# Kernel tuning notes

Measured on AMD Instinct MI355X. Metric: run time of the kernel, lower is better.

The kernel has to match this reference:

```python
import jax, jax.numpy as jnp
import numpy as np

D = 512
H = 8
HD = D // H  # 64
B = 16
N = 64        # seq_len (variable nodes)
S = N + 1     # new_seq (with CLS)
THRESHOLD = 0.5
LN_EPS = 1e-5


def setup_inputs() -> dict:
    key = jax.random.key(0)
    ks = jax.random.split(key, 12)
    s = 0.02
    return {
        "desc_embeddings": jax.random.normal(ks[0], (B, N, D), jnp.float32),
        "name_value_embeddings": jax.random.normal(ks[1], (B, S, D), jnp.float32),
        "w_gt": jax.random.normal(ks[2], (D, D), jnp.float32) * s,
        "b_gt": jnp.zeros((D,), jnp.float32),
        "topology_bias": jnp.zeros((1,), jnp.float32),
        "w_edge1": jax.random.normal(ks[3], (2 * D, D), jnp.float32) * s,
        "b_edge1": jnp.zeros((D,), jnp.float32),
        "ln_gamma": jnp.ones((D,), jnp.float32),
        "ln_beta": jnp.zeros((D,), jnp.float32),
        "w_edge2": jax.random.normal(ks[4], (D, D), jnp.float32) * s,
        "b_edge2": jnp.zeros((D,), jnp.float32),
        "w_q": jax.random.normal(ks[5], (D, D), jnp.float32) * s,
        "b_q": jnp.zeros((D,), jnp.float32),
        "w_k": jax.random.normal(ks[6], (D, D), jnp.float32) * s,
        "b_k": jnp.zeros((D,), jnp.float32),
        "w_v": jax.random.normal(ks[7], (D, D), jnp.float32) * s,
        "b_v": jnp.zeros((D,), jnp.float32),
        "w_attn": jax.random.normal(ks[8], (3 * HD,), jnp.float32) * s,
        "b_attn": jnp.zeros((1,), jnp.float32),
        "w_out": jax.random.normal(ks[9], (D, D), jnp.float32) * s,
        "b_out": jnp.zeros((D,), jnp.float32),
    }


def _layernorm(x, gamma, beta):
    mu = jnp.mean(x, axis=-1, keepdims=True)
    var = jnp.mean(jnp.square(x - mu), axis=-1, keepdims=True)
    return (x - mu) * jax.lax.rsqrt(var + LN_EPS) * gamma + beta


def reference(desc_embeddings, name_value_embeddings, w_gt, b_gt, topology_bias,
              w_edge1, b_edge1, ln_gamma, ln_beta, w_edge2, b_edge2,
              w_q, b_q, w_k, b_k, w_v, b_v, w_attn, b_attn, w_out, b_out):
    b, s, d = name_value_embeddings.shape
    n = s - 1

    # 1. Global topology (projected desc embeddings, cosine sim, sigmoid)
    de = desc_embeddings @ w_gt + b_gt                                   # [B,N,D]
    de_n = de / jnp.linalg.norm(de, axis=-1, keepdims=True)
    global_sim = jnp.einsum('bnd,bmd->bnm', de_n, de_n)
    gt = jax.nn.sigmoid(global_sim + topology_bias)
    # straight-through threshold (frozen=False)
    hard = (gt > THRESHOLD).astype(gt.dtype)
    gA = hard - jax.lax.stop_gradient(gt) + gt

    # 2. Sample-wise similarity over variable tokens
    var = name_value_embeddings[:, 1:, :]
    var_n = var / jnp.linalg.norm(var, axis=-1, keepdims=True)
    sample_sim = jnp.einsum('bnd,bmd->bnm', var_n, var_n)

    # no self-interaction, then graph-conditioned softmax
    gA = gA * (1.0 - jnp.eye(n, dtype=gt.dtype))[None]
    adjacency = jax.nn.softmax(gA * sample_sim, axis=-1)                 # [B,N,N]

    # 4. Edge attributes [B,S,S,2D] and padded adjacency [B,S,S]
    var_edge = jnp.concatenate([
        jnp.broadcast_to(de[:, :, None, :], (b, n, n, d)),
        jnp.broadcast_to(de[:, None, :, :], (b, n, n, d)),
    ], axis=-1)
    cls_edge = jnp.concatenate([de, de], axis=-1)                        # [B,N,2D]
    edge_attr = jnp.zeros((b, s, s, 2 * d), de.dtype)
    edge_attr = edge_attr.at[:, 1:, 1:].set(var_edge)
    edge_attr = edge_attr.at[:, 0, 1:].set(cls_edge)
    edge_attr = edge_attr.at[:, 1:, 0].set(cls_edge)

    new_adj = jnp.zeros((b, s, s), adjacency.dtype)
    new_adj = new_adj.at[:, 1:, 1:].set(adjacency)
    new_adj = new_adj.at[:, 0, 1:].set(1.0)

    # 5. Attention
    q = (name_value_embeddings @ w_q + b_q).reshape(b, s, H, HD).transpose(0, 2, 1, 3)
    k = (name_value_embeddings @ w_k + b_k).reshape(b, s, H, HD).transpose(0, 2, 1, 3)
    v = (name_value_embeddings @ w_v + b_v).reshape(b, s, H, HD).transpose(0, 2, 1, 3)

    # edge MLP: Linear -> LayerNorm -> ReLU -> Linear
    eu = jax.nn.relu(_layernorm(edge_attr @ w_edge1 + b_edge1, ln_gamma, ln_beta)) @ w_edge2 + b_edge2
    eu = eu.reshape(b, s, s, H, HD)                                      # [B,S,S,H,hd]

    # attn_proj(concat([q_i, k_j, e_ij])) decomposed into three dot products
    wq_a, wk_a, we_a = w_attn[:HD], w_attn[HD:2 * HD], w_attn[2 * HD:]
    score_q = jnp.einsum('bhid,d->bhi', q, wq_a)[:, :, :, None]
    score_k = jnp.einsum('bhjd,d->bhj', k, wk_a)[:, :, None, :]
    # edge features are pre-masked by adjacency; linearity lets us mask the score
    score_e = jnp.einsum('bijhd,d->bhij', eu, we_a) * new_adj[:, None]
    attn = score_q + score_k + score_e + b_attn[0]

    attn = attn + jnp.where(new_adj[:, None] == 0, -1e9, 0.0)
    attn = jax.nn.softmax(attn, axis=-1)                                 # [B,H,S,S]
    # dropout p=0 (eval)

    context = jnp.einsum('bhij,bhjd->bhid', attn, v)
    context = context.transpose(0, 2, 1, 3).reshape(b, s, d)
    output = context @ w_out + b_out
    return output, attn
```

## Files before the change

### kernel.cpp

```cpp
#include <hip/hip_runtime.h>
#include <math.h>


constexpr int kD  = 512;
constexpr int kH  = 8;
constexpr int kHD = 64;
constexpr int kB  = 16;
constexpr int kN  = 64;
constexpr int kS  = 65;

typedef short bf16x8 __attribute__((ext_vector_type(8)));
typedef float f32x4  __attribute__((ext_vector_type(4)));

__device__ __forceinline__ float wsum(float x) {
#pragma unroll
  for (int m = 1; m < 64; m <<= 1) x += __shfl_xor(x, m, 64);
  return x;
}
__device__ __forceinline__ float wmax(float x) {
#pragma unroll
  for (int m = 1; m < 64; m <<= 1) x = fmaxf(x, __shfl_xor(x, m, 64));
  return x;
}
__device__ __forceinline__ float osum(float x) {
  x += __shfl_xor(x, 8, 64);
  x += __shfl_xor(x, 16, 64);
  x += __shfl_xor(x, 32, 64);
  return x;
}

__device__ __forceinline__ unsigned short f2bf(float x) {
  unsigned int u = __builtin_bit_cast(unsigned int, x);
  u += 0x7FFFu + ((u >> 16) & 1u);
  return (unsigned short)(u >> 16);
}
__device__ __forceinline__ float bf2f(unsigned short h) {
  return __builtin_bit_cast(float, ((unsigned int)h) << 16);
}
__device__ __forceinline__ unsigned int pk2(unsigned short a, unsigned short b) {
  return (unsigned int)a | ((unsigned int)b << 16);
}

__global__ __launch_bounds__(256) void conv_w(
    const float* __restrict__ w_q, const float* __restrict__ w_k,
    const float* __restrict__ w_v, const float* __restrict__ w_e1,
    const float* __restrict__ w_o, const float* __restrict__ w_gt,
    unsigned short* __restrict__ wt)
{
  __shared__ float T[32][33];
  const int z = blockIdx.z;
  const float* src = (z == 0) ? w_q : (z == 1) ? w_k : (z == 2) ? w_v
                   : (z == 3) ? w_e1 : (z == 4) ? (w_e1 + 262144)
                   : (z == 5) ? w_o : w_gt;
  unsigned short* hi = wt + (size_t)z * 524288;
  unsigned short* lo = hi + 262144;
  const int n0 = blockIdx.x * 32, k0 = blockIdx.y * 32;
  const int tx = threadIdx.x & 31, ty0 = threadIdx.x >> 5;
#pragma unroll
  for (int it = 0; it < 4; ++it) {
    const int ky = ty0 + it * 8;
    T[ky][tx] = src[(size_t)(k0 + ky) * kD + n0 + tx];
  }
  __syncthreads();
#pragma unroll
  for (int it = 0; it < 4; ++it) {
    const int ny = ty0 + it * 8;
    const float x = T[tx][ny];
    const unsigned short h = f2bf(x);
    hi[(size_t)(n0 + ny) * kD + k0 + tx] = h;
    lo[(size_t)(n0 + ny) * kD + k0 + tx] = f2bf(x - bf2f(h));
  }
}

struct MJob { const float* A; const unsigned short* Wh; const unsigned short* Wl;
              const float* bias; float* C; int M; };
struct MJobs { MJob j[4]; };

__global__ __launch_bounds__(256) void gemm_mfma(
    MJobs jobs, int zNorms,
    const float* __restrict__ deN, const float* __restrict__ nvN,
    float* __restrict__ invde, float* __restrict__ invvar)
{
  if ((int)blockIdx.z == zNorms) {
    const int flat = blockIdx.x + gridDim.x * blockIdx.y;
    const int lane = threadIdx.x & 63;
    const int w = threadIdx.x >> 6;
#pragma unroll
    for (int r = 0; r < 4; ++r) {
      const int wid = flat * 16 + w * 4 + r;
      if (wid >= 2 * kB * kN) break;
      const float* row;
      if (wid < kB * kN) {
        row = deN + (size_t)wid * kD;
      } else {
        const int t = wid - kB * kN;
        row = nvN + ((size_t)(t / kN) * kS + 1 + (t % kN)) * kD;
      }
      const float4* r4 = reinterpret_cast<const float4*>(row) + lane * 2;
      const float4 x0 = r4[0], x1 = r4[1];
      float ss = x0.x * x0.x + x0.y * x0.y + x0.z * x0.z + x0.w * x0.w
               + x1.x * x1.x + x1.y * x1.y + x1.z * x1.z + x1.w * x1.w;
      ss = wsum(ss);
      if (lane == 0) {
        const float inv = 1.f / sqrtf(ss);
        if (wid < kB * kN) invde[wid] = inv; else invvar[wid - kB * kN] = inv;
      }
    }
    return;
  }

  const MJob jb = jobs.j[blockIdx.z];
  __shared__ unsigned short Ah[64][40], Al[64][40], Wh[64][40], Wl[64][40];
  const int tid = threadIdx.x;
  const int lane = tid & 63, wv = tid >> 6;
  const int wr = wv >> 1, wc = wv & 1;
  const int bm = blockIdx.x * 64, bn = blockIdx.y * 64;
  const int sr = tid >> 2, sk = (tid & 3) * 8;
  const bool aok = (bm + sr) < jb.M;
  const float* Ap = jb.A + (size_t)(bm + sr) * kD + sk;
  const unsigned short* Whp = jb.Wh + (size_t)(bn + sr) * kD + sk;
  const unsigned short* Wlp = jb.Wl + (size_t)(bn + sr) * kD + sk;

  const f32x4 zero = {0.f, 0.f, 0.f, 0.f};
  f32x4 acc00 = zero, acc01 = zero, acc10 = zero, acc11 = zero;

  for (int k0 = 0; k0 < kD; k0 += 32) {
    float4 a0 = {0.f, 0.f, 0.f, 0.f}, a1 = {0.f, 0.f, 0.f, 0.f};
    if (aok) {
      a0 = *reinterpret_cast<const float4*>(Ap + k0);
      a1 = *reinterpret_cast<const float4*>(Ap + k0 + 4);
    }
    const uint4 wh4 = *reinterpret_cast<const uint4*>(Whp + k0);
    const uint4 wl4 = *reinterpret_cast<const uint4*>(Wlp + k0);
    const float av[8] = {a0.x, a0.y, a0.z, a0.w, a1.x, a1.y, a1.z, a1.w};
    unsigned short h[8], l[8];
#pragma unroll
    for (int e = 0; e < 8; ++e) {
      h[e] = f2bf(av[e]);
      l[e] = f2bf(av[e] - bf2f(h[e]));
    }
    const uint4 hp = { pk2(h[0], h[1]), pk2(h[2], h[3]), pk2(h[4], h[5]), pk2(h[6], h[7]) };
    const uint4 lp = { pk2(l[0], l[1]), pk2(l[2], l[3]), pk2(l[4], l[5]), pk2(l[6], l[7]) };
    *reinterpret_cast<uint4*>(&Ah[sr][sk]) = hp;
    *reinterpret_cast<uint4*>(&Al[sr][sk]) = lp;
    *reinterpret_cast<uint4*>(&Wh[sr][sk]) = wh4;
    *reinterpret_cast<uint4*>(&Wl[sr][sk]) = wl4;
    __syncthreads();

    const int fr = lane & 15, kg = lane >> 4;
#pragma unroll
    for (int fm = 0; fm < 2; ++fm) {
      const int arow = wr * 32 + fm * 16 + fr;
      const bf16x8 amh = *reinterpret_cast<const bf16x8*>(&Ah[arow][kg * 8]);
      const bf16x8 aml = *reinterpret_cast<const bf16x8*>(&Al[arow][kg * 8]);
#pragma unroll
      for (int fn = 0; fn < 2; ++fn) {
        const int wrow = wc * 32 + fn * 16 + fr;
        const bf16x8 bh = *reinterpret_cast<const bf16x8*>(&Wh[wrow][kg * 8]);
        const bf16x8 bl = *reinterpret_cast<const bf16x8*>(&Wl[wrow][kg * 8]);
        f32x4 acc = (fm == 0) ? (fn == 0 ? acc00 : acc01) : (fn == 0 ? acc10 : acc11);
        acc = __builtin_amdgcn_mfma_f32_16x16x32_bf16(amh, bh, acc, 0, 0, 0);
        acc = __builtin_amdgcn_mfma_f32_16x16x32_bf16(amh, bl, acc, 0, 0, 0);
        acc = __builtin_amdgcn_mfma_f32_16x16x32_bf16(aml, bh, acc, 0, 0, 0);
        if (fm == 0) { if (fn == 0) acc00 = acc; else acc01 = acc; }
        else         { if (fn == 0) acc10 = acc; else acc11 = acc; }
      }
    }
    __syncthreads();
  }

  const int rg = lane >> 4, cc = lane & 15;
#pragma unroll
  for (int fm = 0; fm < 2; ++fm) {
#pragma unroll
    for (int fn = 0; fn < 2; ++fn) {
      const f32x4 acc = (fm == 0) ? (fn == 0 ? acc00 : acc01) : (fn == 0 ? acc10 : acc11);
      const int row0 = bm + wr * 32 + fm * 16 + rg * 4;
      const int col  = bn + wc * 32 + fn * 16 + cc;
      const float bb = jb.bias ? jb.bias[col] : 0.f;
#pragma unroll
      for (int e = 0; e < 4; ++e) {
        const int row = row0 + e;
        if (row < jb.M) jb.C[(size_t)row * kD + col] = acc[e] + bb;
      }
    }
  }
}

__global__ __launch_bounds__(512) void graph_prep(
    const float* __restrict__ de, const float* __restrict__ nv,
    const float* __restrict__ invde, const float* __restrict__ invvar,
    const float* __restrict__ topo_p, float* __restrict__ adj,
    const float* __restrict__ q, const float* __restrict__ k,
    const float* __restrict__ w_attn,
    float* __restrict__ sq, float* __restrict__ sk,
    const float* __restrict__ w_edge2, const float* __restrict__ b_edge2,
    unsigned short* __restrict__ w2ph, unsigned short* __restrict__ w2pl,
    float* __restrict__ b2eff)
{
  const int blk = blockIdx.x;
  if (blk < kB * kN) {
    __shared__ float lg[kN];
    const int b = blk >> 6, i = blk & 63;
    const int w = threadIdx.x >> 6, lane = threadIdx.x & 63;
    const int p = lane & 7, oct = lane >> 3;
    const int j = w * 8 + p;
    const float topo = topo_p[0];
    const float4* di = reinterpret_cast<const float4*>(de + ((size_t)b * kN + i) * kD + oct * 64);
    const float4* dj = reinterpret_cast<const float4*>(de + ((size_t)b * kN + j) * kD + oct * 64);
    const float4* vi = reinterpret_cast<const float4*>(nv + ((size_t)b * kS + 1 + i) * kD + oct * 64);
    const float4* vj = reinterpret_cast<const float4*>(nv + ((size_t)b * kS + 1 + j) * kD + oct * 64);
    float g = 0.f, sv = 0.f;
#pragma unroll
    for (int t = 0; t < 16; ++t) {
      const float4 a = di[t], c = dj[t];
      g += a.x * c.x + a.y * c.y + a.z * c.z + a.w * c.w;
      const float4 x = vi[t], y = vj[t];
      sv += x.x * y.x + x.y * y.y + x.z * y.z + x.w * y.w;
    }
    g = osum(g);
    sv = osum(sv);
    if (oct == 0) {
      const float gs = g * invde[b * kN + i] * invde[b * kN + j] + topo;
      const bool hard = (gs > 0.f) && (j != i);
      lg[j] = hard ? sv * invvar[b * kN + i] * invvar[b * kN + j] : 0.f;
    }
    __syncthreads();
    if (threadIdx.x < 64) {
      const float x = lg[lane];
      const float m = wmax(x);
      const float e = expf(x - m);
      const float s = wsum(e);
      adj[((size_t)b * kN + i) * kN + lane] = e / s;
    }
    return;
  }
  if (blk < kB * kN + 33) {
    const int t = (blk - kB * kN) * 512 + threadIdx.x;
    const int total = kB * kS * kH;
    if (t >= 2 * total) return;
    const int which = (t >= total) ? 1 : 0;
    const int r = which ? t - total : t;
    const int h = r % kH, bs = r / kH;
    const float* src = which ? k : q;
    const float* wa = w_attn + which * kHD;
    const float4* row = reinterpret_cast<const float4*>(src + (size_t)bs * kD + h * kHD);
    const float4* w4 = reinterpret_cast<const float4*>(wa);
    float acc = 0.f;
#pragma unroll
    for (int c = 0; c < kHD / 4; ++c) {
      const float4 a = row[c], w = w4[c];
      acc += a.x * w.x + a.y * w.y + a.z * w.z + a.w * w.w;
    }
    (which ? sk : sq)[r] = acc;
    return;
  }
  {
    const int rel = blk - (kB * kN + 33);
    const float4* wa4 = reinterpret_cast<const float4*>(w_attn + 2 * kHD);
    if (rel < 8) {
      const int t = rel * 512 + threadIdx.x;
      const int c = t >> 3, h = t & 7;
      const float4* s4 = reinterpret_cast<const float4*>(w_edge2 + (size_t)c * kD + h * kHD);
      float acc = 0.f;
#pragma unroll
      for (int u = 0; u < kHD / 4; ++u) {
        const float4 a = s4[u], w = wa4[u];
        acc += a.x * w.x + a.y * w.y + a.z * w.z + a.w * w.w;
      }
      const unsigned short hi = f2bf(acc);
      w2ph[h * kD + c] = hi;
      w2pl[h * kD + c] = f2bf(acc - bf2f(hi));
    } else {
      if (threadIdx.x < kH) {
        const int h = threadIdx.x;
        float acc = 0.f;
        for (int d = 0; d < kHD; ++d)
          acc += b_edge2[h * kHD + d] * w_attn[2 * kHD + d];
        b2eff[h] = acc;
      }
      for (int u = threadIdx.x; u < 8 * kD; u += 512) {
        w2ph[8 * kD + u] = 0;
        w2pl[8 * kD + u] = 0;
      }
    }
  }
}

__global__ __launch_bounds__(256) void edge_scores(
    const float* __restrict__ Pp, const float* __restrict__ Qq,
    const float* __restrict__ gamma, const float* __restrict__ beta,
    const unsigned short* __restrict__ w2ph, const unsigned short* __restrict__ w2pl,
    const float* __restrict__ b2eff, float* __restrict__ es)
{
  const int g = blockIdx.x * 4 + (threadIdx.x >> 6);
  const int lane = threadIdx.x & 63;
  const int m = lane & 15, kg = lane >> 4;
  const int base = g * 16;
  const int b = base / (kS * kN);
  const int r0 = base % (kS * kN);
  const int i = r0 / kN, j0 = r0 % kN;
  const int jj = j0 + m;
  const int qrow = b * kN + jj;
  const int prow = (i == 0) ? qrow : (b * kN + i - 1);
  const float* Pr = Pp + (size_t)prow * kD;
  const float* Qr = Qq + (size_t)qrow * kD;

  float s1 = 0.f, s2 = 0.f;
#pragma unroll 4
  for (int s = 0; s < 16; ++s) {
    const int c = s * 32 + kg * 8;
    const float4 pa = *reinterpret_cast<const float4*>(Pr + c);
    const float4 pb = *reinterpret_cast<const float4*>(Pr + c + 4);
    const float4 qa = *reinterpret_cast<const float4*>(Qr + c);
    const float4 qb = *reinterpret_cast<const float4*>(Qr + c + 4);
    const float z0 = pa.x + qa.x, z1 = pa.y + qa.y, z2 = pa.z + qa.z, z3 = pa.w + qa.w;
    const float z4 = pb.x + qb.x, z5 = pb.y + qb.y, z6 = pb.z + qb.z, z7 = pb.w + qb.w;
    s1 += ((z0 + z1) + (z2 + z3)) + ((z4 + z5) + (z6 + z7));
    s2 += ((z0 * z0 + z1 * z1) + (z2 * z2 + z3 * z3))
        + ((z4 * z4 + z5 * z5) + (z6 * z6 + z7 * z7));
  }
  s1 += __shfl_xor(s1, 16, 64); s1 += __shfl_xor(s1, 32, 64);
  s2 += __shfl_xor(s2, 16, 64); s2 += __shfl_xor(s2, 32, 64);
  const float mu = s1 * (1.f / kD);
  const float var = s2 * (1.f / kD) - mu * mu;
  const float rstd = rsqrtf(var + 1e-5f);
  const float nb = -mu * rstd;

  const f32x4 zero = {0.f, 0.f, 0.f, 0.f};
  f32x4 accA = zero, accB = zero, accC = zero;
#pragma unroll 4
  for (int s = 0; s < 16; ++s) {
    const int c = s * 32 + kg * 8;
    const float4 pa = *reinterpret_cast<const float4*>(Pr + c);
    const float4 pb = *reinterpret_cast<const float4*>(Pr + c + 4);
    const float4 qa = *reinterpret_cast<const float4*>(Qr + c);
    const float4 qb = *reinterpret_cast<const float4*>(Qr + c + 4);
    const float4 ga = *reinterpret_cast<const float4*>(gamma + c);
    const float4 gb = *reinterpret_cast<const float4*>(gamma + c + 4);
    const float4 ba = *reinterpret_cast<const float4*>(beta + c);
    const float4 bb = *reinterpret_cast<const float4*>(beta + c + 4);
    const float zv[8] = { pa.x + qa.x, pa.y + qa.y, pa.z + qa.z, pa.w + qa.w,
                          pb.x + qb.x, pb.y + qb.y, pb.z + qb.z, pb.w + qb.w };
    const float gv[8] = { ga.x, ga.y, ga.z, ga.w, gb.x, gb.y, gb.z, gb.w };
    const float bv[8] = { ba.x, ba.y, ba.z, ba.w, bb.x, bb.y, bb.z, bb.w };
    unsigned short h8[8], l8[8];
#pragma unroll
    for (int e = 0; e < 8; ++e) {
      const float zn = fmaf(zv[e], rstd, nb);
      const float eu = fmaxf(fmaf(zn, gv[e], bv[e]), 0.f);
      h8[e] = f2bf(eu);
      l8[e] = f2bf(eu - bf2f(h8[e]));
    }
    const uint4 hp = { pk2(h8[0], h8[1]), pk2(h8[2], h8[3]), pk2(h8[4], h8[5]), pk2(h8[6], h8[7]) };
    const uint4 lp = { pk2(l8[0], l8[1]), pk2(l8[2], l8[3]), pk2(l8[4], l8[5]), pk2(l8[6], l8[7]) };
    const bf16x8 Af_h = __builtin_bit_cast(bf16x8, hp);
    const bf16x8 Af_l = __builtin_bit_cast(bf16x8, lp);
    const bf16x8 Bh = *reinterpret_cast<const bf16x8*>(w2ph + (size_t)m * kD + c);
    const bf16x8 Bl = *reinterpret_cast<const bf16x8*>(w2pl + (size_t)m * kD + c);
    accA = __builtin_amdgcn_mfma_f32_16x16x32_bf16(Af_h, Bh, accA, 0, 0, 0);
    accB = __builtin_amdgcn_mfma_f32_16x16x32_bf16(Af_h, Bl, accB, 0, 0, 0);
    accC = __builtin_amdgcn_mfma_f32_16x16x32_bf16(Af_l, Bh, accC, 0, 0, 0);
  }

  const int n = lane & 15;
  if (n < kH) {
    const float be = b2eff[n];
#pragma unroll
    for (int e = 0; e < 4; ++e) {
      const int mp = kg * 4 + e;
      es[(((size_t)b * kS + i) * kS + (j0 + mp + 1)) * kH + n]
          = (accA[e] + accB[e]) + accC[e] + be;
    }
  }
}

__global__ __launch_bounds__(576) void attn_ctx(
    const float* __restrict__ sq, const float* __restrict__ sk,
    const float* __restrict__ es, const float* __restrict__ adj,
    const float* __restrict__ v, const float* __restrict__ b_attn,
    float* __restrict__ attn_out, float* __restrict__ ctx)
{
  __shared__ float prob[kH][kS];
  const int bi = blockIdx.x;
  const int b = bi / kS, i = bi % kS;
  const int tid = threadIdx.x;
  const float ba = b_attn[0];
  if (tid < kH * kS) {
    const int h = tid / kS, j = tid % kS;
    float lgv;
    if (j == 0) {
      lgv = -1e30f;
    } else {
      const float a = (i == 0) ? 1.f : adj[((size_t)b * kN + (i - 1)) * kN + (j - 1)];
      lgv = sq[(b * kS + i) * kH + h] + sk[(b * kS + j) * kH + h]
          + es[(((size_t)b * kS + i) * kS + j) * kH + h] * a + ba;
    }
    prob[h][j] = lgv;
  }
  __syncthreads();
  const int w = tid >> 6, lane = tid & 63;
  if (w < kH) {
    const float x = prob[w][lane];
    const float xe = prob[w][64];
    float m = wmax(x);
    m = fmaxf(m, xe);
    const float e = expf(x - m);
    const float ee = expf(xe - m);
    const float s = wsum(e) + ee;
    const float inv = 1.f / s;
    prob[w][lane] = e * inv;
    if (lane == 0) prob[w][64] = ee * inv;
  }
  __syncthreads();
  if (tid < kH * kS) {
    const int h = tid / kS, j = tid % kS;
    attn_out[(((size_t)b * kH + h) * kS + i) * kS + j] = prob[h][j];
  }
  if (tid < kD) {
    const int h = tid >> 6, d = tid & 63;
    const float* vb = v + (size_t)b * kS * kD + h * kHD + d;
    float a0 = 0.f, a1 = 0.f, a2 = 0.f, a3 = 0.f;
#pragma unroll 4
    for (int j = 1; j < kS; j += 4) {
      a0 = fmaf(prob[h][j + 0], vb[(size_t)(j + 0) * kD], a0);
      a1 = fmaf(prob[h][j + 1], vb[(size_t)(j + 1) * kD], a1);
      a2 = fmaf(prob[h][j + 2], vb[(size_t)(j + 2) * kD], a2);
      a3 = fmaf(prob[h][j + 3], vb[(size_t)(j + 3) * kD], a3);
    }
    ctx[((size_t)b * kS + i) * kD + tid] = (a0 + a1) + (a2 + a3);
  }
}

extern "C" void kernel_launch(void* const* d_in, const int* in_sizes, int n_in,
                              void* d_out, int out_size, void* d_ws, size_t ws_size,
                              hipStream_t stream)
{
  const float* desc = (const float*)d_in[0];
  const float* nv   = (const float*)d_in[1];
  const float* w_gt = (const float*)d_in[2];
  const float* b_gt = (const float*)d_in[3];
  const float* topo = (const float*)d_in[4];
  const float* w_e1 = (const float*)d_in[5];
  const float* b_e1 = (const float*)d_in[6];
  const float* ln_g = (const float*)d_in[7];
  const float* ln_b = (const float*)d_in[8];
  const float* w_e2 = (const float*)d_in[9];
  const float* b_e2 = (const float*)d_in[10];
  const float* w_q  = (const float*)d_in[11];
  const float* b_q  = (const float*)d_in[12];
  const float* w_k  = (const float*)d_in[13];
  const float* b_k  = (const float*)d_in[14];
  const float* w_v  = (const float*)d_in[15];
  const float* b_v  = (const float*)d_in[16];
  const float* w_at = (const float*)d_in[17];
  const float* b_at = (const float*)d_in[18];
  const float* w_o  = (const float*)d_in[19];
  const float* b_o  = (const float*)d_in[20];

  float* ws  = (float*)d_ws;
  float* de  = ws;
  float* q   = de  + 524288;
  float* k   = q   + 532480;
  float* v   = k   + 532480;
  float* Pp  = v   + 532480;
  float* Qq  = Pp  + 524288;
  float* adj = Qq  + 524288;
  float* sq  = adj + 65536;
  float* sk  = sq  + 8320;
  float* es  = sk  + 8320;
  float* ctx = es  + 540800;
  float* b2e = ctx + 532480;
  float* ivd = b2e + 8;
  float* ivv = ivd + 1024;
  unsigned short* wt   = (unsigned short*)(ivv + 1024);
  unsigned short* w2ph = wt + 7u * 524288;
  unsigned short* w2pl = w2ph + 8192;

  float* out  = (float*)d_out;
  float* attn = out + (size_t)kB * kS * kD;

  conv_w<<<dim3(16, 16, 7), 256, 0, stream>>>(w_q, w_k, w_v, w_e1, w_o, w_gt, wt);
  {
    MJobs jobs;
    jobs.j[0] = { desc, wt + 6u * 524288, wt + 6u * 524288 + 262144, b_gt, de, kB * kN };
    jobs.j[1] = { nv,   wt + 0u * 524288, wt + 0u * 524288 + 262144, b_q,  q,  kB * kS };
    jobs.j[2] = { nv,   wt + 1u * 524288, wt + 1u * 524288 + 262144, b_k,  k,  kB * kS };
    jobs.j[3] = { nv,   wt + 2u * 524288, wt + 2u * 524288 + 262144, b_v,  v,  kB * kS };
    gemm_mfma<<<dim3(17, 8, 4), 256, 0, stream>>>(jobs, -1, nullptr, nullptr, nullptr, nullptr);
  }
  {
    MJobs jobs;
    jobs.j[0] = { de, wt + 3u * 524288, wt + 3u * 524288 + 262144, b_e1,   Pp, kB * kN };
    jobs.j[1] = { de, wt + 4u * 524288, wt + 4u * 524288 + 262144, nullptr, Qq, kB * kN };
    jobs.j[2] = jobs.j[0]; jobs.j[3] = jobs.j[0];
    gemm_mfma<<<dim3(16, 8, 3), 256, 0, stream>>>(jobs, 2, de, nv, ivd, ivv);
  }
  graph_prep<<<1066, 512, 0, stream>>>(de, nv, ivd, ivv, topo, adj,
                                       q, k, w_at, sq, sk,
                                       w_e2, b_e2, w2ph, w2pl, b2e);
  edge_scores<<<1040, 256, 0, stream>>>(Pp, Qq, ln_g, ln_b, w2ph, w2pl, b2e, es);
  attn_ctx<<<kB * kS, 576, 0, stream>>>(sq, sk, es, adj, v, b_at, attn, ctx);
  {
    MJobs jobs;
    jobs.j[0] = { ctx, wt + 5u * 524288, wt + 5u * 524288 + 262144, b_o, out, kB * kS };
    jobs.j[1] = jobs.j[0]; jobs.j[2] = jobs.j[0]; jobs.j[3] = jobs.j[0];
    gemm_mfma<<<dim3(17, 8, 1), 256, 0, stream>>>(jobs, -1, nullptr, nullptr, nullptr, nullptr);
  }
}
```

Baseline: 300.6 us.

## Precompute LayerNorm statistics algebraically and split edge-score K across two waves

The per-edge LayerNorm mean and variance are no longer recomputed by reading both 512-wide rows. Row sums and sums of squares of P and Q, plus the P·Q cross dot products, are precomputed in new graph_prep blocks, and the statistics are assembled algebraically from them. edge_scores now splits the K dimension across two waves per tile and combines the partial MFMA results through shared memory. This removes a full extra pass over the P/Q rows per edge, in exchange for extra prep blocks and a block-level barrier. The one-pass variance formula may lose some precision.

```diff
diff --git a/kernel.cpp b/kernel.cpp
--- a/kernel.cpp
+++ b/kernel.cpp
@@ -196,7 +196,11 @@
     float* __restrict__ sq, float* __restrict__ sk,
     const float* __restrict__ w_edge2, const float* __restrict__ b_edge2,
     unsigned short* __restrict__ w2ph, unsigned short* __restrict__ w2pl,
-    float* __restrict__ b2eff)
+    float* __restrict__ b2eff,
+    const float* __restrict__ Pp, const float* __restrict__ Qq,
+    float* __restrict__ s1p, float* __restrict__ s2p,
+    float* __restrict__ s1q, float* __restrict__ s2q,
+    float* __restrict__ pqd)
 {
   const int blk = blockIdx.x;
   if (blk < kB * kN) {
@@ -255,7 +259,7 @@
     (which ? sk : sq)[r] = acc;
     return;
   }
-  {
+  if (blk < kB * kN + 33 + 9) {
     const int rel = blk - (kB * kN + 33);
     const float4* wa4 = reinterpret_cast<const float4*>(w_attn + 2 * kHD);
     if (rel < 8) {
@@ -284,6 +288,47 @@
         w2pl[8 * kD + u] = 0;
       }
     }
+    return;
+  }
+  if (blk < kB * kN + 33 + 9 + 128) {
+    const int rel = blk - (kB * kN + 33 + 9);
+    const int w = threadIdx.x >> 6, lane = threadIdx.x & 63;
+#pragma unroll
+    for (int pass = 0; pass < 2; ++pass) {
+      const int rid = rel * 16 + w * 2 + pass;
+      const float* row = (rid < kB * kN) ? (Pp + (size_t)rid * kD)
+                                         : (Qq + (size_t)(rid - kB * kN) * kD);
+      const float4* r4 = reinterpret_cast<const float4*>(row) + lane * 2;
+      const float4 x0 = r4[0], x1 = r4[1];
+      float s = ((x0.x + x0.y) + (x0.z + x0.w)) + ((x1.x + x1.y) + (x1.z + x1.w));
+      float ss = (x0.x * x0.x + x0.y * x0.y + x0.z * x0.z + x0.w * x0.w)
+               + (x1.x * x1.x + x1.y * x1.y + x1.z * x1.z + x1.w * x1.w);
+      s = wsum(s);
+      ss = wsum(ss);
+      if (lane == 0) {
+        if (rid < kB * kN) { s1p[rid] = s; s2p[rid] = ss; }
+        else               { s1q[rid - kB * kN] = s; s2q[rid - kB * kN] = ss; }
+      }
+    }
+    return;
+  }
+  {
+    const int rel = blk - (kB * kN + 33 + 9 + 128);
+    const int b = rel >> 6, ip = rel & 63;
+    const int w = threadIdx.x >> 6, lane = threadIdx.x & 63;
+    const int p = lane & 7, oct = lane >> 3;
+    const int j = w * 8 + p;
+    const float4* Pr = reinterpret_cast<const float4*>(Pp + ((size_t)(b * kN + ip)) * kD + oct * 64);
+    const float4* Qr = reinterpret_cast<const float4*>(Qq + ((size_t)(b * kN + j)) * kD + oct * 64);
+    float d = 0.f;
+#pragma unroll
+    for (int t = 0; t < 16; ++t) {
+      const float4 a = Pr[t], c = Qr[t];
+      d += a.x * c.x + a.y * c.y + a.z * c.z + a.w * c.w;
+    }
+    d = osum(d);
+    if (oct == 0)
+      pqd[(size_t)(b * kN + ip) * kN + j] = d;
   }
 }
 
@@ -291,11 +336,18 @@
     const float* __restrict__ Pp, const float* __restrict__ Qq,
     const float* __restrict__ gamma, const float* __restrict__ beta,
     const unsigned short* __restrict__ w2ph, const unsigned short* __restrict__ w2pl,
-    const float* __restrict__ b2eff, float* __restrict__ es)
+    const float* __restrict__ b2eff,
+    const float* __restrict__ s1p, const float* __restrict__ s2p,
+    const float* __restrict__ s1q, const float* __restrict__ s2q,
+    const float* __restrict__ pqd, float* __restrict__ es)
 {
-  const int g = blockIdx.x * 4 + (threadIdx.x >> 6);
-  const int lane = threadIdx.x & 63;
+  __shared__ float sh[2][64][4];
+  const int tid = threadIdx.x;
+  const int wv = tid >> 6;
+  const int pg = wv >> 1, half = wv & 1;
+  const int lane = tid & 63;
   const int m = lane & 15, kg = lane >> 4;
+  const int g = blockIdx.x * 2 + pg;
   const int base = g * 16;
   const int b = base / (kS * kN);
   const int r0 = base % (kS * kN);
@@ -303,35 +355,23 @@
   const int jj = j0 + m;
   const int qrow = b * kN + jj;
   const int prow = (i == 0) ? qrow : (b * kN + i - 1);
-  const float* Pr = Pp + (size_t)prow * kD;
-  const float* Qr = Qq + (size_t)qrow * kD;
-
-  float s1 = 0.f, s2 = 0.f;
-#pragma unroll 4
-  for (int s = 0; s < 16; ++s) {
-    const int c = s * 32 + kg * 8;
-    const float4 pa = *reinterpret_cast<const float4*>(Pr + c);
-    const float4 pb = *reinterpret_cast<const float4*>(Pr + c + 4);
-    const float4 qa = *reinterpret_cast<const float4*>(Qr + c);
-    const float4 qb = *reinterpret_cast<const float4*>(Qr + c + 4);
-    const float z0 = pa.x + qa.x, z1 = pa.y + qa.y, z2 = pa.z + qa.z, z3 = pa.w + qa.w;
-    const float z4 = pb.x + qb.x, z5 = pb.y + qb.y, z6 = pb.z + qb.z, z7 = pb.w + qb.w;
-    s1 += ((z0 + z1) + (z2 + z3)) + ((z4 + z5) + (z6 + z7));
-    s2 += ((z0 * z0 + z1 * z1) + (z2 * z2 + z3 * z3))
-        + ((z4 * z4 + z5 * z5) + (z6 * z6 + z7 * z7));
-  }
-  s1 += __shfl_xor(s1, 16, 64); s1 += __shfl_xor(s1, 32, 64);
-  s2 += __shfl_xor(s2, 16, 64); s2 += __shfl_xor(s2, 32, 64);
+
+  const float s1 = s1p[prow] + s1q[qrow];
+  const float s2 = s2p[prow] + 2.f * pqd[(size_t)prow * kN + jj] + s2q[qrow];
   const float mu = s1 * (1.f / kD);
   const float var = s2 * (1.f / kD) - mu * mu;
   const float rstd = rsqrtf(var + 1e-5f);
   const float nb = -mu * rstd;
 
+  const float* Pr = Pp + (size_t)prow * kD;
+  const float* Qr = Qq + (size_t)qrow * kD;
+  const int cbase = half * 256;
+
   const f32x4 zero = {0.f, 0.f, 0.f, 0.f};
   f32x4 accA = zero, accB = zero, accC = zero;
-#pragma unroll 4
-  for (int s = 0; s < 16; ++s) {
-    const int c = s * 32 + kg * 8;
+#pragma unroll
+  for (int s = 0; s < 8; ++s) {
+    const int c = cbase + s * 32 + kg * 8;
     const float4 pa = *reinterpret_cast<const float4*>(Pr + c);
     const float4 pb = *reinterpret_cast<const float4*>(Pr + c + 4);
     const float4 qa = *reinterpret_cast<const float4*>(Qr + c);
@@ -363,14 +403,25 @@
     accC = __builtin_amdgcn_mfma_f32_16x16x32_bf16(Af_l, Bh, accC, 0, 0, 0);
   }
 
-  const int n = lane & 15;
-  if (n < kH) {
-    const float be = b2eff[n];
-#pragma unroll
-    for (int e = 0; e < 4; ++e) {
-      const int mp = kg * 4 + e;
-      es[(((size_t)b * kS + i) * kS + (j0 + mp + 1)) * kH + n]
-          = (accA[e] + accB[e]) + accC[e] + be;
+  float acc[4];
+#pragma unroll
+  for (int e = 0; e < 4; ++e) acc[e] = (accA[e] + accB[e]) + accC[e];
+
+  if (half == 1) {
+#pragma unroll
+    for (int e = 0; e < 4; ++e) sh[pg][lane][e] = acc[e];
+  }
+  __syncthreads();
+  if (half == 0) {
+    const int n = lane & 15;
+    if (n < kH) {
+      const float be = b2eff[n];
+#pragma unroll
+      for (int e = 0; e < 4; ++e) {
+        const int mp = kg * 4 + e;
+        es[(((size_t)b * kS + i) * kS + (j0 + mp + 1)) * kH + n]
+            = acc[e] + sh[pg][lane][e] + be;
+      }
     }
   }
 }
@@ -473,7 +524,12 @@
   float* b2e = ctx + 532480;
   float* ivd = b2e + 8;
   float* ivv = ivd + 1024;
-  unsigned short* wt   = (unsigned short*)(ivv + 1024);
+  float* s1p = ivv + 1024;
+  float* s2p = s1p + 1024;
+  float* s1q = s2p + 1024;
+  float* s2q = s1q + 1024;
+  float* pqd = s2q + 1024;
+  unsigned short* wt   = (unsigned short*)(pqd + 65536);
   unsigned short* w2ph = wt + 7u * 524288;
   unsigned short* w2pl = w2ph + 8192;
 
@@ -496,10 +552,12 @@
     jobs.j[2] = jobs.j[0]; jobs.j[3] = jobs.j[0];
     gemm_mfma<<<dim3(16, 8, 3), 256, 0, stream>>>(jobs, 2, de, nv, ivd, ivv);
   }
-  graph_prep<<<1066, 512, 0, stream>>>(de, nv, ivd, ivv, topo, adj,
+  graph_prep<<<2218, 512, 0, stream>>>(de, nv, ivd, ivv, topo, adj,
                                        q, k, w_at, sq, sk,
-                                       w_e2, b_e2, w2ph, w2pl, b2e);
-  edge_scores<<<1040, 256, 0, stream>>>(Pp, Qq, ln_g, ln_b, w2ph, w2pl, b2e, es);
+                                       w_e2, b_e2, w2ph, w2pl, b2e,
+                                       Pp, Qq, s1p, s2p, s1q, s2q, pqd);
+  edge_scores<<<2080, 256, 0, stream>>>(Pp, Qq, ln_g, ln_b, w2ph, w2pl, b2e,
+                                        s1p, s2p, s1q, s2q, pqd, es);
   attn_ctx<<<kB * kS, 576, 0, stream>>>(sq, sk, es, adj, v, b_at, attn, ctx);
   {
     MJobs jobs;
```

Measured after the change: 288.9 us. -3.9%, faster.
